# Performance work log

Measured on AMD Instinct MI355X. Metric: run time of the kernel, lower is better.

Reference implementation:

```python
import jax, jax.numpy as jnp
import numpy as np

B, T, D = 4096, 200, 64
H0, H1 = 128, 64
NEG = float(-2**32 + 1)  # tf padding value


def setup_inputs() -> dict:
    key = jax.random.key(0)
    ks = jax.random.split(key, 8)
    q = jax.random.normal(ks[0], (B, D), dtype=jnp.float32)
    k = jax.random.normal(ks[1], (B, T, D), dtype=jnp.float32)
    v = jax.random.normal(ks[2], (B, T, D), dtype=jnp.float32)
    mask = jax.random.randint(ks[3], (B, T), 0, 2).astype(jnp.int32)
    W0 = jax.random.normal(ks[4], (4 * D, H0), dtype=jnp.float32) * (1.0 / np.sqrt(4 * D))
    b0 = jnp.zeros((H0,), dtype=jnp.float32)
    W1 = jax.random.normal(ks[5], (H0, H1), dtype=jnp.float32) * (1.0 / np.sqrt(H0))
    b1 = jnp.zeros((H1,), dtype=jnp.float32)
    Wf = jax.random.normal(ks[6], (H1, 1), dtype=jnp.float32) * (1.0 / np.sqrt(H1))
    bf = jnp.zeros((1,), dtype=jnp.float32)
    return {"q": q, "k": k, "v": v, "mask": mask,
            "W0": W0, "b0": b0, "W1": W1, "b1": b1, "Wf": Wf, "bf": bf}


def reference(q, k, v, mask, W0, b0, W1, b1, Wf, bf):
    # tile q across history positions: [B, D] -> [B, T, D]
    qt = jnp.broadcast_to(q[:, None, :], k.shape)
    # DIN interaction features: [B, T, 4D]
    info = jnp.concatenate([qt, k, qt - k, qt * k], axis=-1)
    # small scorer MLP (Dense+relu, Dense+relu, Dense(1))
    h = jax.nn.relu(jnp.einsum('btf,fh->bth', info, W0) + b0)
    h = jax.nn.relu(jnp.einsum('btf,fh->bth', h, W1) + b1)
    logits = (jnp.einsum('btf,fh->bth', h, Wf) + bf)[..., 0]  # [B, T]
    # mask then softmax over history
    logits = jnp.where(mask == 0, NEG, logits)
    att = jax.nn.softmax(logits, axis=-1)  # [B, T]
    # weighted pooling: [B, T] x [B, T, D] -> [B, D]
    return jnp.einsum('bt,btd->bd', att, v)
```

## Files before the change

kernel.cpp:

```cpp
#include <hip/hip_runtime.h>

typedef __attribute__((ext_vector_type(4))) _Float16 f16x4;
typedef __attribute__((ext_vector_type(8))) _Float16 f16x8;
typedef __attribute__((ext_vector_type(4))) float f32x4;

#define NB 4096
#define TT 200
#define DD 64
#define H0 128
#define H1 64
#define MP 72
#define WP 136

#define WS_BC 0
#define WS_DD 16384
#define WS_W1 32768
#define WS_CB 50176

__global__ __launch_bounds__(256)
void pre_fold(const float* __restrict__ W0, const float* __restrict__ W1,
              unsigned char* __restrict__ ws)
{
  int idx = blockIdx.x * 256 + threadIdx.x;
  _Float16* bcT  = (_Float16*)(ws + WS_BC);
  _Float16* ddT  = (_Float16*)(ws + WS_DD);
  _Float16* w1p  = (_Float16*)(ws + WS_W1);
  if (idx < 8192) {
    int h = idx >> 6, d = idx & 63;
    bcT[h * 64 + d] = (_Float16)(W0[(64 + d) * H0 + h] - W0[(128 + d) * H0 + h]);
    ddT[h * 64 + d] = (_Float16)(W0[(192 + d) * H0 + h]);
  } else {
    int i = idx - 8192;
    int jrow = i >> 7, p = i & 127;
    int m = p >> 5, g4p = (p >> 3) & 3, jj = p & 7;
    int h = 32 * m + 16 * (jj >> 2) + 4 * g4p + (jj & 3);
    w1p[jrow * WP + p] = (_Float16)W1[h * H1 + jrow];
  }
}

__global__ __launch_bounds__(256)
void pre_cb(const float* __restrict__ q, const float* __restrict__ W0,
            const float* __restrict__ b0, unsigned char* __restrict__ ws)
{
  __shared__ float WacS[DD * H0];
  __shared__ float qS2[2][DD];
  const int tid = threadIdx.x;
  float* cb = (float*)(ws + WS_CB);

  #pragma unroll 4
  for (int i = 0; i < 32; ++i) {
    int idx = i * 256 + tid;
    int d = idx >> 7, h = idx & 127;
    WacS[idx] = W0[d * H0 + h] + W0[(128 + d) * H0 + h];
  }
  __syncthreads();

  const int half = tid >> 7, h = tid & 127;
  #pragma unroll 1
  for (int p = 0; p < 16; ++p) {
    int bpair = blockIdx.x * 32 + p * 2;
    if (tid < DD) qS2[0][tid] = q[(size_t)bpair * DD + tid];
    else if (tid >= 128 && tid < 128 + DD) qS2[1][tid - 128] = q[(size_t)(bpair + 1) * DD + (tid - 128)];
    __syncthreads();
    float s = b0[h];
    #pragma unroll 8
    for (int d = 0; d < DD; ++d) s = fmaf(qS2[half][d], WacS[d * H0 + h], s);
    cb[(size_t)(bpair + half) * H0 + h] = s;
    __syncthreads();
  }
}

__global__ __launch_bounds__(256, 4)
void din_attn(const float* __restrict__ q, const float* __restrict__ k,
              const float* __restrict__ v, const int* __restrict__ mask,
              const float* __restrict__ b1, const float* __restrict__ Wf,
              const unsigned char* __restrict__ ws, float* __restrict__ out)
{
  const int b    = blockIdx.x;
  const int tid  = threadIdx.x;
  const int lane = tid & 63;
  const int wid  = tid >> 6;
  const int r16  = lane & 15;
  const int g4   = lane >> 4;

  __shared__ __align__(16) _Float16 MhT[H0 * MP];
  __shared__ __align__(16) _Float16 W1p[H1 * WP];
  __shared__ float qS[DD];
  __shared__ float cbS[H0];
  __shared__ float b1S[H1];
  __shared__ float WfS[H1];
  __shared__ float sP[208];
  __shared__ int   sM[TT];
  __shared__ float red[8];
  __shared__ float pool[256];

  const float* qb = q + b * DD;
  const float* kb = k + (size_t)b * TT * DD;
  const float* vb = v + (size_t)b * TT * DD;
  const int*   mb = mask + b * TT;

  {
    const uint4* src = (const uint4*)(ws + WS_W1);
    uint4* dst = (uint4*)W1p;
    #pragma unroll
    for (int i = 0; i < 5; ++i) {
      int idx = i * 256 + tid;
      if (idx < (H1 * WP * 2) / 16) dst[idx] = src[idx];
    }
  }
  if (tid < DD) qS[tid] = qb[tid];
  if (tid < TT) sM[tid] = mb[tid];
  if (tid < H0) cbS[tid] = ((const float*)(ws + WS_CB))[(size_t)b * H0 + tid];
  if (tid >= H0 && tid < H0 + H1) b1S[tid - H0] = b1[tid - H0];
  if (tid >= H0 + H1 && tid < H0 + 2 * H1) WfS[tid - H0 - H1] = Wf[tid - H0 - H1];
  __syncthreads();

  {
    const _Float16* bcT = (const _Float16*)(ws + WS_BC);
    const _Float16* ddT = (const _Float16*)(ws + WS_DD);
    const int dblk = (tid & 7) * 8;
    const int h4 = (tid >> 3) * 4;
    float q8[8];
    #pragma unroll
    for (int j = 0; j < 8; ++j) q8[j] = qS[dblk + j];
    #pragma unroll
    for (int hi = 0; hi < 4; ++hi) {
      const int h = h4 + hi;
      f16x8 bc8 = *(const f16x8*)(bcT + h * 64 + dblk);
      f16x8 dd8 = *(const f16x8*)(ddT + h * 64 + dblk);
      f16x8 o8;
      #pragma unroll
      for (int j = 0; j < 8; ++j)
        o8[j] = (_Float16)((float)bc8[j] + q8[j] * (float)dd8[j]);
      *(f16x8*)(&MhT[h * MP + dblk]) = o8;
    }
  }

  const int dof = 8 * g4;
  float4 kq[4];
  {
    const int trow = wid * 16 + r16;
    kq[0] = *(const float4*)(kb + trow * DD + dof);
    kq[1] = *(const float4*)(kb + trow * DD + dof + 4);
    kq[2] = *(const float4*)(kb + trow * DD + 32 + dof);
    kq[3] = *(const float4*)(kb + trow * DD + 32 + dof + 4);
  }
  __syncthreads();

  #pragma unroll 1
  for (int s = wid; s < 13; s += 4) {
    const int t0   = s * 16;
    const int trow = t0 + r16;
    int mm = (trow < TT) ? sM[trow] : -1;

    f16x8 bh0, bh1;
    {
      float f0[8] = {kq[0].x, kq[0].y, kq[0].z, kq[0].w,
                     kq[1].x, kq[1].y, kq[1].z, kq[1].w};
      float f1[8] = {kq[2].x, kq[2].y, kq[2].z, kq[2].w,
                     kq[3].x, kq[3].y, kq[3].z, kq[3].w};
      #pragma unroll
      for (int j = 0; j < 8; ++j) {
        bh0[j] = (_Float16)f0[j];
        bh1[j] = (_Float16)f1[j];
      }
    }
    const int sn = s + 4;
    if (sn < 13) {
      const int trn = sn * 16 + r16;
      if (trn < TT) {
        kq[0] = *(const float4*)(kb + trn * DD + dof);
        kq[1] = *(const float4*)(kb + trn * DD + dof + 4);
        kq[2] = *(const float4*)(kb + trn * DD + 32 + dof);
        kq[3] = *(const float4*)(kb + trn * DD + 32 + dof + 4);
      } else {
        float4 z = {0.f, 0.f, 0.f, 0.f};
        kq[0] = z; kq[1] = z; kq[2] = z; kq[3] = z;
      }
    }

    f32x4 acc1[4];
    #pragma unroll
    for (int c1 = 0; c1 < 4; ++c1) acc1[c1] = (f32x4){0.f, 0.f, 0.f, 0.f};

    #pragma unroll 1
    for (int m = 0; m < 4; ++m) {
      const _Float16* rowE = &MhT[((2 * m) * 16 + r16) * MP];
      const _Float16* rowO = rowE + 16 * MP;
      f16x8 afE0 = *(const f16x8*)(rowE + dof);
      f16x8 afE1 = *(const f16x8*)(rowE + 32 + dof);
      f32x4 a0e = {0.f, 0.f, 0.f, 0.f};
      a0e = __builtin_amdgcn_mfma_f32_16x16x32_f16(afE0, bh0, a0e, 0, 0, 0);
      a0e = __builtin_amdgcn_mfma_f32_16x16x32_f16(afE1, bh1, a0e, 0, 0, 0);
      f16x8 afO0 = *(const f16x8*)(rowO + dof);
      f16x8 afO1 = *(const f16x8*)(rowO + 32 + dof);
      f32x4 a0o = {0.f, 0.f, 0.f, 0.f};
      a0o = __builtin_amdgcn_mfma_f32_16x16x32_f16(afO0, bh0, a0o, 0, 0, 0);
      a0o = __builtin_amdgcn_mfma_f32_16x16x32_f16(afO1, bh1, a0o, 0, 0, 0);

      f32x4 cbe = *(const f32x4*)(&cbS[(2 * m) * 16 + 4 * g4]);
      f32x4 cbo = *(const f32x4*)(&cbS[(2 * m) * 16 + 16 + 4 * g4]);
      f16x8 hf;
      #pragma unroll
      for (int r = 0; r < 4; ++r) {
        float he = a0e[r] + cbe[r];
        float ho = a0o[r] + cbo[r];
        hf[r]     = (_Float16)(he > 0.f ? he : 0.f);
        hf[4 + r] = (_Float16)(ho > 0.f ? ho : 0.f);
      }
      #pragma unroll
      for (int c1 = 0; c1 < 4; ++c1) {
        f16x8 af1 = *(const f16x8*)(&W1p[(c1 * 16 + r16) * WP + m * 32 + dof]);
        acc1[c1] = __builtin_amdgcn_mfma_f32_16x16x32_f16(af1, hf, acc1[c1], 0, 0, 0);
      }
    }

    float p = 0.f;
    #pragma unroll
    for (int c1 = 0; c1 < 4; ++c1) {
      f32x4 b14 = *(const f32x4*)(&b1S[c1 * 16 + 4 * g4]);
      f32x4 wf4 = *(const f32x4*)(&WfS[c1 * 16 + 4 * g4]);
      #pragma unroll
      for (int r = 0; r < 4; ++r) {
        float h1 = acc1[c1][r] + b14[r];
        h1 = h1 > 0.f ? h1 : 0.f;
        p = fmaf(h1, wf4[r], p);
      }
    }

    p += __shfl_xor(p, 16, 64);
    p += __shfl_xor(p, 32, 64);
    p = (mm == 1) ? p : (mm == 0 ? -1e30f : -2e30f);
    if (g4 == 0) sP[t0 + r16] = p;
  }
  __syncthreads();

  const int tg = lane >> 4;
  const int dq = lane & 15;
  const int tbase = wid * 52;
  f32x4 vv[13];
  #pragma unroll
  for (int i = 0; i < 13; ++i) {
    int t = tbase + i * 4 + tg;
    int tc = t < TT ? t : TT - 1;
    vv[i] = *(const f32x4*)(vb + tc * DD + dq * 4);
  }

  float rcpS;
  {
    float val = (tid < 208) ? sP[tid] : -3e30f;
    float mx = val;
    #pragma unroll
    for (int off = 32; off >= 1; off >>= 1) mx = fmaxf(mx, __shfl_xor(mx, off, 64));
    if (lane == 0) red[wid] = mx;
    __syncthreads();
    float M = fmaxf(fmaxf(red[0], red[1]), fmaxf(red[2], red[3]));
    float e = (tid < 208) ? __expf(val - M) : 0.f;
    float se = e;
    #pragma unroll
    for (int off = 32; off >= 1; off >>= 1) se += __shfl_xor(se, off, 64);
    if (lane == 0) red[4 + wid] = se;
    __syncthreads();
    rcpS = 1.f / ((red[4] + red[5]) + (red[6] + red[7]));
    if (tid < 208) sP[tid] = e;
  }
  __syncthreads();

  {
    f32x4 o4 = {0.f, 0.f, 0.f, 0.f};
    #pragma unroll
    for (int i = 0; i < 13; ++i) {
      int t = tbase + i * 4 + tg;
      float w = (t < TT) ? sP[t] : 0.f;
      #pragma unroll
      for (int j = 0; j < 4; ++j) o4[j] = fmaf(w, vv[i][j], o4[j]);
    }
    #pragma unroll
    for (int j = 0; j < 4; ++j) {
      o4[j] += __shfl_xor(o4[j], 16, 64);
      o4[j] += __shfl_xor(o4[j], 32, 64);
    }
    if (tg == 0) *(f32x4*)(&pool[wid * 64 + dq * 4]) = o4;
  }
  __syncthreads();

  if (tid < DD)
    out[b * DD + tid] = ((pool[tid] + pool[64 + tid])
                       + (pool[128 + tid] + pool[192 + tid])) * rcpS;
}

extern "C" void kernel_launch(void* const* d_in, const int* in_sizes, int n_in,
                              void* d_out, int out_size, void* d_ws, size_t ws_size,
                              hipStream_t stream) {
  const float* q    = (const float*)d_in[0];
  const float* k    = (const float*)d_in[1];
  const float* v    = (const float*)d_in[2];
  const int*   mask = (const int*)d_in[3];
  const float* W0   = (const float*)d_in[4];
  const float* b0   = (const float*)d_in[5];
  const float* W1   = (const float*)d_in[6];
  const float* b1   = (const float*)d_in[7];
  const float* Wf   = (const float*)d_in[8];
  float* out = (float*)d_out;
  unsigned char* ws = (unsigned char*)d_ws;

  pre_fold<<<dim3(64), dim3(256), 0, stream>>>(W0, W1, ws);
  pre_cb<<<dim3(128), dim3(256), 0, stream>>>(q, W0, b0, ws);
  din_attn<<<dim3(NB), dim3(256), 0, stream>>>(q, k, v, mask, b1, Wf, ws, out);
}
```

Measured before the change: 124.3 us.

## Replace padded LDS layouts with XOR-swizzled layouts and read mask directly

Drops the padding rows (MP=72, WP=136) on the MhT and W1p shared-memory tiles and uses XOR swizzles on the 8-element column groups to avoid bank conflicts. pre_fold writes W1 into the matching swizzled order, which shrinks the workspace and moves the cb offset. The mask is now read from global memory inside the loop instead of being staged in LDS. The smaller LDS footprint could allow higher occupancy, at the cost of extra index arithmetic and a global load per tile.

```diff
diff --git a/kernel.cpp b/kernel.cpp
--- a/kernel.cpp
+++ b/kernel.cpp
@@ -9,13 +9,11 @@
 #define DD 64
 #define H0 128
 #define H1 64
-#define MP 72
-#define WP 136
 
 #define WS_BC 0
 #define WS_DD 16384
 #define WS_W1 32768
-#define WS_CB 50176
+#define WS_CB 49152
 
 __global__ __launch_bounds__(256)
 void pre_fold(const float* __restrict__ W0, const float* __restrict__ W1,
@@ -34,7 +32,8 @@
     int jrow = i >> 7, p = i & 127;
     int m = p >> 5, g4p = (p >> 3) & 3, jj = p & 7;
     int h = 32 * m + 16 * (jj >> 2) + 4 * g4p + (jj & 3);
-    w1p[jrow * WP + p] = (_Float16)W1[h * H1 + jrow];
+    int up = p >> 3, wi = p & 7;
+    w1p[jrow * 128 + (((up ^ (jrow & 15)) << 3) | wi)] = (_Float16)W1[h * H1 + jrow];
   }
 }
 
@@ -83,14 +82,13 @@
   const int r16  = lane & 15;
   const int g4   = lane >> 4;
 
-  __shared__ __align__(16) _Float16 MhT[H0 * MP];
-  __shared__ __align__(16) _Float16 W1p[H1 * WP];
+  __shared__ __align__(16) _Float16 MhT[H0 * 64];
+  __shared__ __align__(16) _Float16 W1p[H1 * 128];
   __shared__ float qS[DD];
   __shared__ float cbS[H0];
   __shared__ float b1S[H1];
   __shared__ float WfS[H1];
   __shared__ float sP[208];
-  __shared__ int   sM[TT];
   __shared__ float red[8];
   __shared__ float pool[256];
 
@@ -103,13 +101,9 @@
     const uint4* src = (const uint4*)(ws + WS_W1);
     uint4* dst = (uint4*)W1p;
     #pragma unroll
-    for (int i = 0; i < 5; ++i) {
-      int idx = i * 256 + tid;
-      if (idx < (H1 * WP * 2) / 16) dst[idx] = src[idx];
-    }
+    for (int i = 0; i < 4; ++i) dst[i * 256 + tid] = src[i * 256 + tid];
   }
   if (tid < DD) qS[tid] = qb[tid];
-  if (tid < TT) sM[tid] = mb[tid];
   if (tid < H0) cbS[tid] = ((const float*)(ws + WS_CB))[(size_t)b * H0 + tid];
   if (tid >= H0 && tid < H0 + H1) b1S[tid - H0] = b1[tid - H0];
   if (tid >= H0 + H1 && tid < H0 + 2 * H1) WfS[tid - H0 - H1] = Wf[tid - H0 - H1];
@@ -118,7 +112,8 @@
   {
     const _Float16* bcT = (const _Float16*)(ws + WS_BC);
     const _Float16* ddT = (const _Float16*)(ws + WS_DD);
-    const int dblk = (tid & 7) * 8;
+    const int u    = tid & 7;
+    const int dblk = u * 8;
     const int h4 = (tid >> 3) * 4;
     float q8[8];
     #pragma unroll
@@ -132,7 +127,7 @@
       #pragma unroll
       for (int j = 0; j < 8; ++j)
         o8[j] = (_Float16)((float)bc8[j] + q8[j] * (float)dd8[j]);
-      *(f16x8*)(&MhT[h * MP + dblk]) = o8;
+      *(f16x8*)(&MhT[h * 64 + ((u ^ (h & 7)) << 3)]) = o8;
     }
   }
 
@@ -147,11 +142,14 @@
   }
   __syncthreads();
 
+  const int k8 = r16 & 7;
+  const int kW = r16;
+
   #pragma unroll 1
   for (int s = wid; s < 13; s += 4) {
     const int t0   = s * 16;
     const int trow = t0 + r16;
-    int mm = (trow < TT) ? sM[trow] : -1;
+    int mm = (trow < TT) ? mb[trow] : -1;
 
     f16x8 bh0, bh1;
     {
@@ -185,15 +183,15 @@
 
     #pragma unroll 1
     for (int m = 0; m < 4; ++m) {
-      const _Float16* rowE = &MhT[((2 * m) * 16 + r16) * MP];
-      const _Float16* rowO = rowE + 16 * MP;
-      f16x8 afE0 = *(const f16x8*)(rowE + dof);
-      f16x8 afE1 = *(const f16x8*)(rowE + 32 + dof);
+      const _Float16* rowE = &MhT[((2 * m) * 16 + r16) * 64];
+      const _Float16* rowO = rowE + 16 * 64;
+      f16x8 afE0 = *(const f16x8*)(rowE + ((g4 ^ k8) << 3));
+      f16x8 afE1 = *(const f16x8*)(rowE + (((g4 + 4) ^ k8) << 3));
       f32x4 a0e = {0.f, 0.f, 0.f, 0.f};
       a0e = __builtin_amdgcn_mfma_f32_16x16x32_f16(afE0, bh0, a0e, 0, 0, 0);
       a0e = __builtin_amdgcn_mfma_f32_16x16x32_f16(afE1, bh1, a0e, 0, 0, 0);
-      f16x8 afO0 = *(const f16x8*)(rowO + dof);
-      f16x8 afO1 = *(const f16x8*)(rowO + 32 + dof);
+      f16x8 afO0 = *(const f16x8*)(rowO + ((g4 ^ k8) << 3));
+      f16x8 afO1 = *(const f16x8*)(rowO + (((g4 + 4) ^ k8) << 3));
       f32x4 a0o = {0.f, 0.f, 0.f, 0.f};
       a0o = __builtin_amdgcn_mfma_f32_16x16x32_f16(afO0, bh0, a0o, 0, 0, 0);
       a0o = __builtin_amdgcn_mfma_f32_16x16x32_f16(afO1, bh1, a0o, 0, 0, 0);
@@ -210,7 +208,8 @@
       }
       #pragma unroll
       for (int c1 = 0; c1 < 4; ++c1) {
-        f16x8 af1 = *(const f16x8*)(&W1p[(c1 * 16 + r16) * WP + m * 32 + dof]);
+        f16x8 af1 = *(const f16x8*)(&W1p[(c1 * 16 + r16) * 128
+                                         + (((4 * m + g4) ^ kW) << 3)]);
         acc1[c1] = __builtin_amdgcn_mfma_f32_16x16x32_f16(af1, hf, acc1[c1], 0, 0, 0);
       }
     }
```

After: 122.0 us. About the same (-1.9%).
